# Kernel tuning notes

Hardware: AMD Instinct MI355X
Metric: run time of the kernel (lower is better)

Reference implementation:

```python
import math
import jax, jax.numpy as jnp
import numpy as np

B, S, H, O = 16, 2048, 512, 16


def setup_inputs() -> dict:
    key = jax.random.key(0)
    ks = jax.random.split(key, 8)
    ops = jax.random.normal(ks[7], (S, O), dtype=jnp.float32)
    ops = ops.at[:, 0].set(1.0)  # identity operator (frozen ones)
    return {
        "x": jax.random.normal(ks[0], (B, S, H), dtype=jnp.float32),
        "Wv": jax.random.normal(ks[1], (H, H), dtype=jnp.float32) * 0.02,
        "bv": jax.random.normal(ks[2], (H,), dtype=jnp.float32) * 0.02,
        "Wk": jax.random.normal(ks[3], (H, H), dtype=jnp.float32) * 0.02,
        "bk": jax.random.normal(ks[4], (H,), dtype=jnp.float32) * 0.02,
        "Wq_op": jax.random.normal(ks[5], (H, S), dtype=jnp.float32) * 0.02,
        "bq_op": jax.random.normal(ks[6], (H,), dtype=jnp.float32) * 0.02,
        "operators": ops,
    }


def reference(x, Wv, bv, Wk, bk, Wq_op, bq_op, operators):
    # operator_queries[o] = Linear(S->H)(operator_o)  -> [O, H]
    operator_queries = jnp.einsum('so,hs->oh', operators, Wq_op) + bq_op

    values = x @ Wv.T + bv          # [B, S, H]
    keys = x @ Wk.T + bk            # [B, S, H]

    # single shared key-query logits (original computes it twice identically)
    logits = jnp.einsum('bsh,oh->bso', keys, operator_queries) / math.sqrt(H)

    # relevance softmax over sequence positions s
    relevance_weights = jax.nn.softmax(logits, axis=1)  # [B, S, O]

    # per-operator weighted reduce over s, fused: [B, O, H]
    operator_outputs = jnp.einsum('bsh,bso,so->boh', values, relevance_weights, operators)

    # operator-mixing softmax over operators o
    operator_weights = jax.nn.softmax(logits, axis=-1)  # [B, S, O]

    output = jnp.einsum('bso,boh->bsh', operator_weights, operator_outputs)
    return output, operator_queries
```

## Files before the change

kernel.cpp:

```cpp
#include <hip/hip_runtime.h>

#define BB 16
#define SS 2048
#define HH 512
#define ON 16
#define INV_SQRT_H 0.04419417382415922f

#define WKO_OFF 0
#define C_OFF   8192
#define L_OFF   8208
#define TT_OFF  8464
#define G_OFF   8720
#define ZERO_N  139792
#define OO_OFF  139792
#define OQT_OFF 270864
#define LG_OFF  279056

__global__ __launch_bounds__(256) void k_oq(const float* __restrict__ Wq,
                                            const float* __restrict__ bq,
                                            const float* __restrict__ ops,
                                            float* __restrict__ ws,
                                            float* __restrict__ oq_out) {
  const int h = blockIdx.x;
  const int t = threadIdx.x;
  float4 acc[4];
  #pragma unroll
  for (int m = 0; m < 4; ++m) acc[m] = make_float4(0.f, 0.f, 0.f, 0.f);
  for (int s = t; s < SS; s += 256) {
    float wq = Wq[(size_t)h * SS + s];
    const float4* op4 = reinterpret_cast<const float4*>(ops + (size_t)s * ON);
    #pragma unroll
    for (int m = 0; m < 4; ++m) {
      float4 v = op4[m];
      acc[m].x += wq * v.x; acc[m].y += wq * v.y;
      acc[m].z += wq * v.z; acc[m].w += wq * v.w;
    }
  }
  __shared__ float red[256][ON];
  #pragma unroll
  for (int m = 0; m < 4; ++m) {
    red[t][4*m+0] = acc[m].x; red[t][4*m+1] = acc[m].y;
    red[t][4*m+2] = acc[m].z; red[t][4*m+3] = acc[m].w;
  }
  __syncthreads();
  for (int st = 128; st > 0; st >>= 1) {
    if (t < st) {
      #pragma unroll
      for (int o = 0; o < ON; ++o) red[t][o] += red[t + st][o];
    }
    __syncthreads();
  }
  if (t < ON) {
    float v = red[0][t] + bq[h];
    oq_out[(size_t)t * HH + h] = v;
    ws[OQT_OFF + (size_t)h * ON + t] = v;
  }
}

__global__ __launch_bounds__(256) void k_wko(const float* __restrict__ Wk,
                                             const float* __restrict__ bk,
                                             float* __restrict__ ws) {
  const int o = blockIdx.x;
  const int hc = blockIdx.y;
  const int t = threadIdx.x;
  const float* __restrict__ oqT = ws + OQT_OFF;
  const int h0 = hc * 64;
  float acc0 = 0.f, acc1 = 0.f;
  for (int h = h0; h < h0 + 64; ++h) {
    float q = oqT[(size_t)h * ON + o];
    acc0 += q * Wk[(size_t)h * HH + t];
    acc1 += q * Wk[(size_t)h * HH + t + 256];
  }
  unsafeAtomicAdd(&ws[WKO_OFF + (size_t)o * HH + t], acc0);
  unsafeAtomicAdd(&ws[WKO_OFF + (size_t)o * HH + t + 256], acc1);
  if (t == 0) {
    float cp = 0.f;
    for (int h = h0; h < h0 + 64; ++h) cp += bk[h] * oqT[(size_t)h * ON + o];
    unsafeAtomicAdd(&ws[C_OFF + o], cp);
  }
}

__global__ __launch_bounds__(256) void k_main(const float* __restrict__ x,
                                              const float* __restrict__ ops,
                                              float* __restrict__ ws) {
  const int b = blockIdx.x, sc = blockIdx.y, t = threadIdx.x;
  const int sbase = sc * 32;
  const size_t xbase = ((size_t)b * SS + sbase) * HH;

  __shared__ float red[32][17];
  __shared__ float part[3][32][17];
  __shared__ float el[32][ON];

  const int kq = t >> 6, lane = t & 63;
  const int rg = lane >> 2, oq = lane & 3;
  const int k0 = kq * 128;

  float acc[2][4];
  #pragma unroll
  for (int i = 0; i < 2; ++i)
    #pragma unroll
    for (int j = 0; j < 4; ++j) acc[i][j] = 0.f;

  const float4* __restrict__ wko4 = reinterpret_cast<const float4*>(ws + WKO_OFF);
  #pragma unroll 4
  for (int ch = 0; ch < 32; ++ch) {
    const int kk = k0 + ch * 4;
    float4 xr[2], wr[4];
    #pragma unroll
    for (int i = 0; i < 2; ++i)
      xr[i] = *reinterpret_cast<const float4*>(x + xbase + (size_t)(rg + 16 * i) * HH + kk);
    #pragma unroll
    for (int j = 0; j < 4; ++j)
      wr[j] = wko4[(4 * oq + j) * 128 + (kk >> 2)];
    #pragma unroll
    for (int i = 0; i < 2; ++i)
      #pragma unroll
      for (int j = 0; j < 4; ++j)
        acc[i][j] += xr[i].x * wr[j].x + xr[i].y * wr[j].y
                   + xr[i].z * wr[j].z + xr[i].w * wr[j].w;
  }
  if (kq == 0) {
    #pragma unroll
    for (int i = 0; i < 2; ++i)
      #pragma unroll
      for (int j = 0; j < 4; ++j) red[rg + 16 * i][4 * oq + j] = acc[i][j];
  } else {
    #pragma unroll
    for (int i = 0; i < 2; ++i)
      #pragma unroll
      for (int j = 0; j < 4; ++j) part[kq - 1][rg + 16 * i][4 * oq + j] = acc[i][j];
  }
  __syncthreads();

  if (t < 128) {
    const int r = t >> 2, o4 = (t & 3) * 4;
    float lgv[4];
    #pragma unroll
    for (int j = 0; j < 4; ++j) {
      const int o = o4 + j;
      float s = red[r][o] + part[0][r][o] + part[1][r][o] + part[2][r][o] + ws[C_OFF + o];
      lgv[j] = s * INV_SQRT_H;
    }
    *reinterpret_cast<float4*>(ws + LG_OFF + ((size_t)b * SS + sbase + r) * ON + o4) =
        make_float4(lgv[0], lgv[1], lgv[2], lgv[3]);
    *reinterpret_cast<float4*>(&el[r][o4]) =
        make_float4(__expf(lgv[0]), __expf(lgv[1]), __expf(lgv[2]), __expf(lgv[3]));
  }
  __syncthreads();

  if (t < ON) {
    float sl = 0.f, st = 0.f;
    for (int r = 0; r < 32; ++r) {
      float e = el[r][t];
      sl += e;
      st += e * ops[(size_t)(sbase + r) * ON + t];
    }
    unsafeAtomicAdd(&ws[L_OFF + b * ON + t], sl);
    unsafeAtomicAdd(&ws[TT_OFF + b * ON + t], st);
  }

  float a0[ON], a1[ON];
  #pragma unroll
  for (int o = 0; o < ON; ++o) { a0[o] = 0.f; a1[o] = 0.f; }
  for (int s = 0; s < 32; ++s) {
    const float xv0 = x[xbase + (size_t)s * HH + t];
    const float xv1 = x[xbase + (size_t)s * HH + t + 256];
    const float4* e4 = reinterpret_cast<const float4*>(&el[s][0]);
    #pragma unroll
    for (int g = 0; g < 4; ++g) {
      float4 e = e4[g];
      a0[4*g+0] += e.x * xv0; a1[4*g+0] += e.x * xv1;
      a0[4*g+1] += e.y * xv0; a1[4*g+1] += e.y * xv1;
      a0[4*g+2] += e.z * xv0; a1[4*g+2] += e.z * xv1;
      a0[4*g+3] += e.w * xv0; a1[4*g+3] += e.w * xv1;
    }
  }
  float* G = ws + G_OFF + (size_t)b * ON * HH;
  #pragma unroll
  for (int o = 0; o < ON; ++o) {
    unsafeAtomicAdd(&G[(size_t)o * HH + t], a0[o]);
    unsafeAtomicAdd(&G[(size_t)o * HH + t + 256], a1[o]);
  }
}

__global__ __launch_bounds__(256) void k_oo(const float* __restrict__ Wv,
                                            const float* __restrict__ bv,
                                            float* __restrict__ ws) {
  const int b = blockIdx.x, oqi = blockIdx.y, hqi = blockIdx.z, t = threadIdx.x;
  const int o0 = oqi * 4, h0 = hqi * 128;
  __shared__ float4 Gs[4][128];
  __shared__ float invLs[4], tts[4];
  if (t < 4) {
    float invL = 1.f / ws[L_OFF + b * ON + o0 + t];
    invLs[t] = invL;
    tts[t] = ws[TT_OFF + b * ON + o0 + t] * invL;
  }
  __syncthreads();
  {
    int idx = t;
    #pragma unroll
    for (int p = 0; p < 2; ++p, idx += 256) {
      int oo = idx >> 7, kk = idx & 127;
      float4 g = reinterpret_cast<const float4*>(
          ws + G_OFF + ((size_t)b * ON + o0 + oo) * HH)[kk];
      float sv = invLs[oo];
      Gs[oo][kk] = make_float4(g.x * sv, g.y * sv, g.z * sv, g.w * sv);
    }
  }
  __syncthreads();
  const int hh = h0 + (t & 127);
  const int op = (t >> 7) * 2;
  const float4* __restrict__ wv4 = reinterpret_cast<const float4*>(Wv + (size_t)hh * HH);
  float a0 = 0.f, a1 = 0.f;
  #pragma unroll 4
  for (int kk = 0; kk < 128; ++kk) {
    float4 wv = wv4[kk];
    float4 g0 = Gs[op][kk], g1 = Gs[op + 1][kk];
    a0 += g0.x * wv.x + g0.y * wv.y + g0.z * wv.z + g0.w * wv.w;
    a1 += g1.x * wv.x + g1.y * wv.y + g1.z * wv.z + g1.w * wv.w;
  }
  float* OOp = ws + OO_OFF + ((size_t)b * ON + o0) * HH;
  OOp[(size_t)op * HH + hh]       = a0 + bv[hh] * tts[op];
  OOp[(size_t)(op + 1) * HH + hh] = a1 + bv[hh] * tts[op + 1];
}

__global__ __launch_bounds__(256) void k_out(float* __restrict__ ws,
                                             float* __restrict__ out) {
  const int b = blockIdx.x, sc = blockIdx.y, t = threadIdx.x;
  const int rbase = b * SS + sc * 32;
  __shared__ float wl[32 * ON];

  float4 oo4[ON];
  const float4* __restrict__ OO4 =
      reinterpret_cast<const float4*>(ws + OO_OFF + (size_t)b * ON * HH);
  const int hq = t & 127;
  #pragma unroll
  for (int o = 0; o < ON; ++o) oo4[o] = OO4[o * 128 + hq];

  if (t < 32) {
    const float4* lg4 = reinterpret_cast<const float4*>(ws + LG_OFF + (size_t)(rbase + t) * ON);
    float l[ON];
    float4 p0 = lg4[0], p1 = lg4[1], p2 = lg4[2], p3 = lg4[3];
    l[0]=p0.x; l[1]=p0.y; l[2]=p0.z; l[3]=p0.w;
    l[4]=p1.x; l[5]=p1.y; l[6]=p1.z; l[7]=p1.w;
    l[8]=p2.x; l[9]=p2.y; l[10]=p2.z; l[11]=p2.w;
    l[12]=p3.x; l[13]=p3.y; l[14]=p3.z; l[15]=p3.w;
    float m = l[0];
    #pragma unroll
    for (int o = 1; o < ON; ++o) m = fmaxf(m, l[o]);
    float sum = 0.f;
    #pragma unroll
    for (int o = 0; o < ON; ++o) { l[o] = __expf(l[o] - m); sum += l[o]; }
    float inv = 1.f / sum;
    #pragma unroll
    for (int o = 0; o < ON; ++o) wl[t * ON + o] = l[o] * inv;
  }
  __syncthreads();

  const int rsub = t >> 7;
  const float4* wl4 = reinterpret_cast<const float4*>(wl);
  float4* __restrict__ out4 = reinterpret_cast<float4*>(out);
  for (int i = 0; i < 16; ++i) {
    const int r = rsub * 16 + i;
    float4 w0 = wl4[r * 4 + 0], w1 = wl4[r * 4 + 1], w2 = wl4[r * 4 + 2], w3 = wl4[r * 4 + 3];
    float w[ON];
    w[0]=w0.x; w[1]=w0.y; w[2]=w0.z; w[3]=w0.w;
    w[4]=w1.x; w[5]=w1.y; w[6]=w1.z; w[7]=w1.w;
    w[8]=w2.x; w[9]=w2.y; w[10]=w2.z; w[11]=w2.w;
    w[12]=w3.x; w[13]=w3.y; w[14]=w3.z; w[15]=w3.w;
    float4 v = make_float4(0.f, 0.f, 0.f, 0.f);
    #pragma unroll
    for (int o = 0; o < ON; ++o) {
      v.x += w[o] * oo4[o].x; v.y += w[o] * oo4[o].y;
      v.z += w[o] * oo4[o].z; v.w += w[o] * oo4[o].w;
    }
    out4[(size_t)(rbase + r) * 128 + hq] = v;
  }
}

extern "C" void kernel_launch(void* const* d_in, const int* in_sizes, int n_in,
                              void* d_out, int out_size, void* d_ws, size_t ws_size,
                              hipStream_t stream) {
  const float* x   = (const float*)d_in[0];
  const float* Wv  = (const float*)d_in[1];
  const float* bv  = (const float*)d_in[2];
  const float* Wk  = (const float*)d_in[3];
  const float* bk  = (const float*)d_in[4];
  const float* Wq  = (const float*)d_in[5];
  const float* bq  = (const float*)d_in[6];
  const float* ops = (const float*)d_in[7];
  float* out = (float*)d_out;
  float* ws  = (float*)d_ws;
  float* oq_out = out + (size_t)BB * SS * HH;

  hipMemsetAsync(ws, 0, (size_t)ZERO_N * sizeof(float), stream);

  k_oq<<<512, 256, 0, stream>>>(Wq, bq, ops, ws, oq_out);
  k_wko<<<dim3(16, 8), 256, 0, stream>>>(Wk, bk, ws);
  k_main<<<dim3(16, 64), 256, 0, stream>>>(x, ops, ws);
  k_oo<<<dim3(16, 4, 4), 256, 0, stream>>>(Wv, bv, ws);
  k_out<<<dim3(16, 64), 256, 0, stream>>>(ws, out);
}
```

Measured before the change: 245.1 us.

## Replace G atomics with scratch partials plus reduce kernel, transpose Wv, store exps

k_main now writes per-chunk partial G and L/TT sums to scratch (the output buffer, overwritten later) instead of global atomics, and a new k_gred kernel reduces them. Wv is transposed in a merged pre-kernel that also zeroes the workspace in place of a memset. k_oo then reads Wv transposed with coalesced float4 loads. Exponentials are stored once and reused in k_out, so the softmax recompute is dropped, without max subtraction. This removes atomic contention and a launch, at the cost of extra scratch traffic (~32MB written and read) and an extra kernel.

```diff
diff --git a/kernel.cpp b/kernel.cpp
--- a/kernel.cpp
+++ b/kernel.cpp
@@ -8,52 +8,77 @@
 
 #define WKO_OFF 0
 #define C_OFF   8192
+#define ZERO_N  8208
 #define L_OFF   8208
 #define TT_OFF  8464
 #define G_OFF   8720
-#define ZERO_N  139792
-#define OO_OFF  139792
-#define OQT_OFF 270864
-#define LG_OFF  279056
-
-__global__ __launch_bounds__(256) void k_oq(const float* __restrict__ Wq,
-                                            const float* __restrict__ bq,
-                                            const float* __restrict__ ops,
-                                            float* __restrict__ ws,
-                                            float* __restrict__ oq_out) {
-  const int h = blockIdx.x;
+#define OQT_OFF 139792
+#define EL_OFF  147984
+#define OO_OFF  672272
+#define WVT_OFF 803344
+
+#define PG_OFF 0
+#define PL_OFF 8388608
+
+__global__ __launch_bounds__(256) void k_pre(const float* __restrict__ Wv,
+                                             const float* __restrict__ Wq,
+                                             const float* __restrict__ bq,
+                                             const float* __restrict__ ops,
+                                             float* __restrict__ ws,
+                                             float* __restrict__ oq_out) {
+  const int blk = blockIdx.x;
   const int t = threadIdx.x;
-  float4 acc[4];
-  #pragma unroll
-  for (int m = 0; m < 4; ++m) acc[m] = make_float4(0.f, 0.f, 0.f, 0.f);
-  for (int s = t; s < SS; s += 256) {
-    float wq = Wq[(size_t)h * SS + s];
-    const float4* op4 = reinterpret_cast<const float4*>(ops + (size_t)s * ON);
+  __shared__ float tile[32][33];
+  __shared__ float red[256][ON];
+
+  if (blk < 256) {
+    const int tx = t & 31, ty = t >> 5;
+    const int x0 = (blk & 15) * 32, y0 = (blk >> 4) * 32;
+    #pragma unroll
+    for (int j = 0; j < 4; ++j)
+      tile[ty + 8 * j][tx] = Wv[(size_t)(y0 + ty + 8 * j) * HH + x0 + tx];
+    __syncthreads();
+    float* __restrict__ WvT = ws + WVT_OFF;
+    #pragma unroll
+    for (int j = 0; j < 4; ++j)
+      WvT[(size_t)(x0 + ty + 8 * j) * HH + y0 + tx] = tile[tx][ty + 8 * j];
+  } else if (blk < 768) {
+    const int h = blk - 256;
+    float4 acc[4];
+    #pragma unroll
+    for (int m = 0; m < 4; ++m) acc[m] = make_float4(0.f, 0.f, 0.f, 0.f);
+    for (int s = t; s < SS; s += 256) {
+      float wq = Wq[(size_t)h * SS + s];
+      const float4* op4 = reinterpret_cast<const float4*>(ops + (size_t)s * ON);
+      #pragma unroll
+      for (int m = 0; m < 4; ++m) {
+        float4 v = op4[m];
+        acc[m].x += wq * v.x; acc[m].y += wq * v.y;
+        acc[m].z += wq * v.z; acc[m].w += wq * v.w;
+      }
+    }
     #pragma unroll
     for (int m = 0; m < 4; ++m) {
-      float4 v = op4[m];
-      acc[m].x += wq * v.x; acc[m].y += wq * v.y;
-      acc[m].z += wq * v.z; acc[m].w += wq * v.w;
-    }
-  }
-  __shared__ float red[256][ON];
-  #pragma unroll
-  for (int m = 0; m < 4; ++m) {
-    red[t][4*m+0] = acc[m].x; red[t][4*m+1] = acc[m].y;
-    red[t][4*m+2] = acc[m].z; red[t][4*m+3] = acc[m].w;
-  }
-  __syncthreads();
-  for (int st = 128; st > 0; st >>= 1) {
-    if (t < st) {
-      #pragma unroll
-      for (int o = 0; o < ON; ++o) red[t][o] += red[t + st][o];
+      red[t][4*m+0] = acc[m].x; red[t][4*m+1] = acc[m].y;
+      red[t][4*m+2] = acc[m].z; red[t][4*m+3] = acc[m].w;
     }
     __syncthreads();
-  }
-  if (t < ON) {
-    float v = red[0][t] + bq[h];
-    oq_out[(size_t)t * HH + h] = v;
-    ws[OQT_OFF + (size_t)h * ON + t] = v;
+    for (int st = 128; st > 0; st >>= 1) {
+      if (t < st) {
+        #pragma unroll
+        for (int o = 0; o < ON; ++o) red[t][o] += red[t + st][o];
+      }
+      __syncthreads();
+    }
+    if (t < ON) {
+      float v = red[0][t] + bq[h];
+      oq_out[(size_t)t * HH + h] = v;
+      ws[OQT_OFF + (size_t)h * ON + t] = v;
+    }
+  } else {
+    float4 z = make_float4(0.f, 0.f, 0.f, 0.f);
+    float4* z4 = reinterpret_cast<float4*>(ws);
+    for (int i = (blk - 768) * 256 + t; i < ZERO_N / 4; i += 1024) z4[i] = z;
   }
 }
 
@@ -82,7 +107,8 @@
 
 __global__ __launch_bounds__(256) void k_main(const float* __restrict__ x,
                                               const float* __restrict__ ops,
-                                              float* __restrict__ ws) {
+                                              float* __restrict__ ws,
+                                              float* __restrict__ scratch) {
   const int b = blockIdx.x, sc = blockIdx.y, t = threadIdx.x;
   const int sbase = sc * 32;
   const size_t xbase = ((size_t)b * SS + sbase) * HH;
@@ -134,29 +160,28 @@
 
   if (t < 128) {
     const int r = t >> 2, o4 = (t & 3) * 4;
-    float lgv[4];
+    float e[4];
     #pragma unroll
     for (int j = 0; j < 4; ++j) {
       const int o = o4 + j;
       float s = red[r][o] + part[0][r][o] + part[1][r][o] + part[2][r][o] + ws[C_OFF + o];
-      lgv[j] = s * INV_SQRT_H;
-    }
-    *reinterpret_cast<float4*>(ws + LG_OFF + ((size_t)b * SS + sbase + r) * ON + o4) =
-        make_float4(lgv[0], lgv[1], lgv[2], lgv[3]);
-    *reinterpret_cast<float4*>(&el[r][o4]) =
-        make_float4(__expf(lgv[0]), __expf(lgv[1]), __expf(lgv[2]), __expf(lgv[3]));
-  }
-  __syncthreads();
-
-  if (t < ON) {
-    float sl = 0.f, st = 0.f;
-    for (int r = 0; r < 32; ++r) {
-      float e = el[r][t];
-      sl += e;
-      st += e * ops[(size_t)(sbase + r) * ON + t];
-    }
-    unsafeAtomicAdd(&ws[L_OFF + b * ON + t], sl);
-    unsafeAtomicAdd(&ws[TT_OFF + b * ON + t], st);
+      e[j] = __expf(s * INV_SQRT_H);
+    }
+    float4 ev = make_float4(e[0], e[1], e[2], e[3]);
+    *reinterpret_cast<float4*>(ws + EL_OFF + ((size_t)b * SS + sbase + r) * ON + o4) = ev;
+    *reinterpret_cast<float4*>(&el[r][o4]) = ev;
+  }
+  __syncthreads();
+
+  if (t < 32) {
+    const int o = t & 15, which = t >> 4;
+    float s = 0.f;
+    if (which == 0) {
+      for (int r = 0; r < 32; ++r) s += el[r][o];
+    } else {
+      for (int r = 0; r < 32; ++r) s += el[r][o] * ops[(size_t)(sbase + r) * ON + o];
+    }
+    scratch[PL_OFF + (size_t)(b * 64 + sc) * 32 + t] = s;
   }
 
   float a0[ON], a1[ON];
@@ -175,20 +200,43 @@
       a0[4*g+3] += e.w * xv0; a1[4*g+3] += e.w * xv1;
     }
   }
-  float* G = ws + G_OFF + (size_t)b * ON * HH;
+  float* __restrict__ PG = scratch + PG_OFF + (size_t)(b * 64 + sc) * (ON * HH);
   #pragma unroll
   for (int o = 0; o < ON; ++o) {
-    unsafeAtomicAdd(&G[(size_t)o * HH + t], a0[o]);
-    unsafeAtomicAdd(&G[(size_t)o * HH + t + 256], a1[o]);
-  }
-}
-
-__global__ __launch_bounds__(256) void k_oo(const float* __restrict__ Wv,
-                                            const float* __restrict__ bv,
+    PG[(size_t)o * HH + t]       = a0[o];
+    PG[(size_t)o * HH + t + 256] = a1[o];
+  }
+}
+
+__global__ __launch_bounds__(256) void k_gred(const float* __restrict__ scratch,
+                                              float* __restrict__ ws) {
+  const int b = blockIdx.x, og = blockIdx.y, t = threadIdx.x;
+  const int o = og * 2 + (t >> 7), k4 = t & 127;
+  const float4* __restrict__ PG4 =
+      reinterpret_cast<const float4*>(scratch + PG_OFF) + (size_t)b * 64 * 2048;
+  float4 acc = make_float4(0.f, 0.f, 0.f, 0.f);
+  #pragma unroll 8
+  for (int sc = 0; sc < 64; ++sc) {
+    float4 v = PG4[(size_t)sc * 2048 + o * 128 + k4];
+    acc.x += v.x; acc.y += v.y; acc.z += v.z; acc.w += v.w;
+  }
+  reinterpret_cast<float4*>(ws + G_OFF)[(size_t)(b * ON + o) * 128 + k4] = acc;
+
+  if (og == 0 && t < 32) {
+    const float* __restrict__ PL = scratch + PL_OFF + (size_t)b * 64 * 32;
+    float v = 0.f;
+    for (int sc = 0; sc < 64; ++sc) v += PL[sc * 32 + t];
+    if (t < 16) ws[L_OFF + b * ON + t] = v;
+    else        ws[TT_OFF + b * ON + (t - 16)] = v;
+  }
+}
+
+__global__ __launch_bounds__(256) void k_oo(const float* __restrict__ bv,
                                             float* __restrict__ ws) {
   const int b = blockIdx.x, oqi = blockIdx.y, hqi = blockIdx.z, t = threadIdx.x;
-  const int o0 = oqi * 4, h0 = hqi * 128;
-  __shared__ float4 Gs[4][128];
+  const int o0 = oqi * 4;
+  __shared__ float Gs[4][HH];
+  __shared__ float4 rbuf[128];
   __shared__ float invLs[4], tts[4];
   if (t < 4) {
     float invL = 1.f / ws[L_OFF + b * ON + o0 + t];
@@ -197,31 +245,40 @@
   }
   __syncthreads();
   {
-    int idx = t;
-    #pragma unroll
-    for (int p = 0; p < 2; ++p, idx += 256) {
-      int oo = idx >> 7, kk = idx & 127;
-      float4 g = reinterpret_cast<const float4*>(
-          ws + G_OFF + ((size_t)b * ON + o0 + oo) * HH)[kk];
-      float sv = invLs[oo];
-      Gs[oo][kk] = make_float4(g.x * sv, g.y * sv, g.z * sv, g.w * sv);
-    }
-  }
-  __syncthreads();
-  const int hh = h0 + (t & 127);
-  const int op = (t >> 7) * 2;
-  const float4* __restrict__ wv4 = reinterpret_cast<const float4*>(Wv + (size_t)hh * HH);
-  float a0 = 0.f, a1 = 0.f;
-  #pragma unroll 4
-  for (int kk = 0; kk < 128; ++kk) {
-    float4 wv = wv4[kk];
-    float4 g0 = Gs[op][kk], g1 = Gs[op + 1][kk];
-    a0 += g0.x * wv.x + g0.y * wv.y + g0.z * wv.z + g0.w * wv.w;
-    a1 += g1.x * wv.x + g1.y * wv.y + g1.z * wv.z + g1.w * wv.w;
-  }
-  float* OOp = ws + OO_OFF + ((size_t)b * ON + o0) * HH;
-  OOp[(size_t)op * HH + hh]       = a0 + bv[hh] * tts[op];
-  OOp[(size_t)(op + 1) * HH + hh] = a1 + bv[hh] * tts[op + 1];
+    const float4* __restrict__ G4 =
+        reinterpret_cast<const float4*>(ws + G_OFF) + (size_t)(b * ON + o0) * 128;
+    float4* Gs4 = reinterpret_cast<float4*>(&Gs[0][0]);
+    #pragma unroll
+    for (int p = 0; p < 2; ++p) {
+      int i = p * 256 + t;
+      float4 g = G4[i];
+      float sv = invLs[i >> 7];
+      Gs4[i] = make_float4(g.x * sv, g.y * sv, g.z * sv, g.w * sv);
+    }
+  }
+  __syncthreads();
+  const int oo = (t >> 5) & 3;
+  const int ks = t >> 7;
+  const int h4 = hqi * 32 + (t & 31);
+  const float4* __restrict__ WvT4 = reinterpret_cast<const float4*>(ws + WVT_OFF);
+  float4 a = make_float4(0.f, 0.f, 0.f, 0.f);
+  const int kbase = ks * 256;
+  #pragma unroll 8
+  for (int k = 0; k < 256; ++k) {
+    float4 w = WvT4[(size_t)(kbase + k) * 128 + h4];
+    float g = Gs[oo][kbase + k];
+    a.x += g * w.x; a.y += g * w.y; a.z += g * w.z; a.w += g * w.w;
+  }
+  if (ks == 1) rbuf[t - 128] = a;
+  __syncthreads();
+  if (ks == 0) {
+    float4 r2 = rbuf[t];
+    a.x += r2.x; a.y += r2.y; a.z += r2.z; a.w += r2.w;
+    const float tt = tts[oo];
+    const float4 bvv = *reinterpret_cast<const float4*>(bv + h4 * 4);
+    a.x += bvv.x * tt; a.y += bvv.y * tt; a.z += bvv.z * tt; a.w += bvv.w * tt;
+    reinterpret_cast<float4*>(ws + OO_OFF + ((size_t)b * ON + o0 + oo) * HH)[h4] = a;
+  }
 }
 
 __global__ __launch_bounds__(256) void k_out(float* __restrict__ ws,
@@ -238,22 +295,15 @@
   for (int o = 0; o < ON; ++o) oo4[o] = OO4[o * 128 + hq];
 
   if (t < 32) {
-    const float4* lg4 = reinterpret_cast<const float4*>(ws + LG_OFF + (size_t)(rbase + t) * ON);
-    float l[ON];
-    float4 p0 = lg4[0], p1 = lg4[1], p2 = lg4[2], p3 = lg4[3];
-    l[0]=p0.x; l[1]=p0.y; l[2]=p0.z; l[3]=p0.w;
-    l[4]=p1.x; l[5]=p1.y; l[6]=p1.z; l[7]=p1.w;
-    l[8]=p2.x; l[9]=p2.y; l[10]=p2.z; l[11]=p2.w;
-    l[12]=p3.x; l[13]=p3.y; l[14]=p3.z; l[15]=p3.w;
-    float m = l[0];
-    #pragma unroll
-    for (int o = 1; o < ON; ++o) m = fmaxf(m, l[o]);
-    float sum = 0.f;
-    #pragma unroll
-    for (int o = 0; o < ON; ++o) { l[o] = __expf(l[o] - m); sum += l[o]; }
+    const float4* e4 = reinterpret_cast<const float4*>(ws + EL_OFF + (size_t)(rbase + t) * ON);
+    float4 p0 = e4[0], p1 = e4[1], p2 = e4[2], p3 = e4[3];
+    float sum = p0.x + p0.y + p0.z + p0.w + p1.x + p1.y + p1.z + p1.w
+              + p2.x + p2.y + p2.z + p2.w + p3.x + p3.y + p3.z + p3.w;
     float inv = 1.f / sum;
-    #pragma unroll
-    for (int o = 0; o < ON; ++o) wl[t * ON + o] = l[o] * inv;
+    wl[t*ON+ 0] = p0.x*inv; wl[t*ON+ 1] = p0.y*inv; wl[t*ON+ 2] = p0.z*inv; wl[t*ON+ 3] = p0.w*inv;
+    wl[t*ON+ 4] = p1.x*inv; wl[t*ON+ 5] = p1.y*inv; wl[t*ON+ 6] = p1.z*inv; wl[t*ON+ 7] = p1.w*inv;
+    wl[t*ON+ 8] = p2.x*inv; wl[t*ON+ 9] = p2.y*inv; wl[t*ON+10] = p2.z*inv; wl[t*ON+11] = p2.w*inv;
+    wl[t*ON+12] = p3.x*inv; wl[t*ON+13] = p3.y*inv; wl[t*ON+14] = p3.z*inv; wl[t*ON+15] = p3.w*inv;
   }
   __syncthreads();
 
@@ -293,11 +343,10 @@
   float* ws  = (float*)d_ws;
   float* oq_out = out + (size_t)BB * SS * HH;
 
-  hipMemsetAsync(ws, 0, (size_t)ZERO_N * sizeof(float), stream);
-
-  k_oq<<<512, 256, 0, stream>>>(Wq, bq, ops, ws, oq_out);
+  k_pre<<<772, 256, 0, stream>>>(Wv, Wq, bq, ops, ws, oq_out);
   k_wko<<<dim3(16, 8), 256, 0, stream>>>(Wk, bk, ws);
-  k_main<<<dim3(16, 64), 256, 0, stream>>>(x, ops, ws);
-  k_oo<<<dim3(16, 4, 4), 256, 0, stream>>>(Wv, bv, ws);
+  k_main<<<dim3(16, 64), 256, 0, stream>>>(x, ops, ws, out);
+  k_gred<<<dim3(16, 8), 256, 0, stream>>>(out, ws);
+  k_oo<<<dim3(16, 4, 4), 256, 0, stream>>>(bv, ws);
   k_out<<<dim3(16, 64), 256, 0, stream>>>(ws, out);
 }
```

Measured after the change: 232.2 us. 5.3% less time.
